# Kernel optimization log

Hardware: AMD Instinct MI355X
Metric: run time of the kernel (lower is better)

Reference implementation:

```python
import jax, jax.numpy as jnp
import numpy as np

E, H, DK, DV, HID, B, S = 512, 8, 64, 64, 2048, 8, 1024
EPS = 1e-15


def _ln(x, g, b):
    m = x.mean(-1, keepdims=True)
    v = ((x - m) ** 2).mean(-1, keepdims=True)  # unbiased=False
    return g * (x - m) / jnp.sqrt(v + EPS) + b


def _mha(x, kv, Wq, bq, Wk, bk, Wv, bv, Wo, bo, causal):
    # Wq/Wk: [H, DK, E], Wv: [H, DV, E] -- stacked per-head nn.Linear weights
    q = jnp.einsum('bse,hde->bhsd', x, Wq) + bq[None, :, None, :]
    k = jnp.einsum('bte,hde->bhtd', kv, Wk) + bk[None, :, None, :]
    v = jnp.einsum('bte,hde->bhtd', kv, Wv) + bv[None, :, None, :]
    scale = jnp.sqrt(jnp.asarray(q.shape[-1], q.dtype))
    s = jnp.einsum('bhsd,bhtd->bhst', q, k) / scale
    if causal:
        Sq, Tk = s.shape[-2], s.shape[-1]
        mask = jnp.triu(jnp.full((Sq, Tk), -jnp.inf, dtype=s.dtype), k=1)
        s = s + mask[None, None]
    p = jax.nn.softmax(s, axis=-1)
    o = jnp.einsum('bhst,bhtd->bhsd', p, v)
    b_, h_, s_, d_ = o.shape
    o = o.transpose(0, 2, 1, 3).reshape(b_, s_, h_ * d_)
    return o @ Wo.T + bo


def setup_inputs() -> dict:
    key = jax.random.key(0)
    ks = iter(jax.random.split(key, 40))

    def n(shape, s=0.02):
        return jax.random.normal(next(ks), shape, dtype=jnp.float32) * s

    inp = {
        'dec_input': jax.random.normal(next(ks), (B, S, E), dtype=jnp.float32),
        'enc_output': jax.random.normal(next(ks), (B, S, E), dtype=jnp.float32),
        # masked self-attention params
        'Wq1': n((H, DK, E)), 'bq1': jnp.zeros((H, DK), jnp.float32),
        'Wk1': n((H, DK, E)), 'bk1': jnp.zeros((H, DK), jnp.float32),
        'Wv1': n((H, DV, E)), 'bv1': jnp.zeros((H, DV), jnp.float32),
        'Wo1': n((E, H * DV)), 'bo1': jnp.zeros((E,), jnp.float32),
        # cross-attention params
        'Wq2': n((H, DK, E)), 'bq2': jnp.zeros((H, DK), jnp.float32),
        'Wk2': n((H, DK, E)), 'bk2': jnp.zeros((H, DK), jnp.float32),
        'Wv2': n((H, DV, E)), 'bv2': jnp.zeros((H, DV), jnp.float32),
        'Wo2': n((E, H * DV)), 'bo2': jnp.zeros((E,), jnp.float32),
        # feedforward params
        'Wf1': n((HID, E)), 'bf1': jnp.zeros((HID,), jnp.float32),
        'Wf2': n((E, HID)), 'bf2': jnp.zeros((E,), jnp.float32),
        # layer norm params
        'g1': jnp.ones((E,), jnp.float32), 'be1': jnp.zeros((E,), jnp.float32),
        'g2': jnp.ones((E,), jnp.float32), 'be2': jnp.zeros((E,), jnp.float32),
        'g3': jnp.ones((E,), jnp.float32), 'be3': jnp.zeros((E,), jnp.float32),
    }
    return inp


def reference(dec_input, enc_output,
              Wq1, bq1, Wk1, bk1, Wv1, bv1, Wo1, bo1,
              Wq2, bq2, Wk2, bk2, Wv2, bv2, Wo2, bo2,
              Wf1, bf1, Wf2, bf2,
              g1, be1, g2, be2, g3, be3):
    # masked multi-head self-attention + residual + norm
    a = _mha(dec_input, dec_input, Wq1, bq1, Wk1, bk1, Wv1, bv1, Wo1, bo1, True)
    x = _ln(dec_input + a, g1, be1)
    # cross-attention with encoder output + residual + norm
    c = _mha(x, enc_output, Wq2, bq2, Wk2, bk2, Wv2, bv2, Wo2, bo2, False)
    x = _ln(x + c, g2, be2)
    # position-wise feedforward + residual + norm (dropout=0 -> identity)
    f = jax.nn.relu(x @ Wf1.T + bf1) @ Wf2.T + bf2
    return _ln(x + f, g3, be3)
```

## Files before the change

### kernel.cpp

```cpp
#include <hip/hip_runtime.h>
#include <cstddef>

#define EDIM   512
#define HHEADS 8
#define DHEAD  64
#define HIDDIM 2048
#define BATCH  8
#define SEQ    1024
#define MTOK   (BATCH*SEQ)

typedef __bf16 bf16;
typedef __attribute__((ext_vector_type(8))) __bf16 bf16x8;
typedef __attribute__((ext_vector_type(4))) __bf16 bf16x4;
typedef __attribute__((ext_vector_type(4))) float f32x4;

__device__ __forceinline__ void gl_lds16(const bf16* g, bf16* l) {
  __builtin_amdgcn_global_load_lds(
      (const __attribute__((address_space(1))) unsigned int*)g,
      (__attribute__((address_space(3))) unsigned int*)l, 16, 0, 0);
}

struct WPtrs { const float* p[10]; };

__global__ __launch_bounds__(256)
void convert_weights(WPtrs w, bf16* __restrict__ dst) {
  const size_t v = ((size_t)blockIdx.x * 256 + threadIdx.x) * 4;
  const float* src;
  size_t off;
  if (v < 2097152) { src = w.p[v >> 18]; off = v & 262143; }
  else { const size_t v2 = v - 2097152; src = w.p[8 + (v2 >> 20)]; off = v2 & 1048575; }
  const float4 f = *reinterpret_cast<const float4*>(src + off);
  bf16x4 o;
  o[0] = (bf16)f.x; o[1] = (bf16)f.y; o[2] = (bf16)f.z; o[3] = (bf16)f.w;
  *reinterpret_cast<bf16x4*>(dst + v) = o;
}

__global__ __launch_bounds__(256)
void f2b_kernel(const float* __restrict__ src, bf16* __restrict__ dst) {
  const size_t i = (size_t)blockIdx.x * 256 + threadIdx.x;
  const float4 f = reinterpret_cast<const float4*>(src)[i];
  bf16x4 o;
  o[0] = (bf16)f.x; o[1] = (bf16)f.y; o[2] = (bf16)f.z; o[3] = (bf16)f.w;
  reinterpret_cast<bf16x4*>(dst)[i] = o;
}

template<int OM, bool RELU, int BN_>
__global__ __launch_bounds__(256)
void gemm_bf16(const bf16* __restrict__ A, const bf16* __restrict__ W,
               const float* __restrict__ bias, const float* __restrict__ bias2,
               const float* __restrict__ bias3,
               void* __restrict__ C0, void* __restrict__ C1, void* __restrict__ C2,
               float scale, int seg_base, int Ndim, int Kdim) {
  constexpr int WGN = BN_ / 64;
  constexpr int WGM = 4 / WGN;
  constexpr int RPW = 128 / WGM;
  constexpr int MI  = RPW / 16;
  constexpr int NI  = 4;

  __shared__ bf16 As[128 * 32];
  __shared__ bf16 Ws[BN_ * 32];
  const int tid  = threadIdx.x;
  const int lane = tid & 63;
  const int w    = tid >> 6;
  const int wr   = w / WGN, wc = w % WGN;
  const int bm   = blockIdx.y * 128;
  const int bn   = blockIdx.x * BN_;
  const int frow = lane & 15;
  const int fk   = (lane >> 4) * 8;
  const int srow = lane >> 2;
  const int scol = (lane & 3) * 8;

  f32x4 acc[MI][NI] = {};

  const int nsteps = Kdim / 32;
  for (int s = 0; s < nsteps; ++s) {
    const int k0 = s * 32;
    __syncthreads();
    gl_lds16(A + (size_t)(bm + w*16       + srow) * Kdim + k0 + scol, &As[w * 512]);
    gl_lds16(A + (size_t)(bm + (w+4)*16   + srow) * Kdim + k0 + scol, &As[(w+4) * 512]);
    gl_lds16(W + (size_t)(bn + w*16       + srow) * Kdim + k0 + scol, &Ws[w * 512]);
    if (BN_ == 128)
      gl_lds16(W + (size_t)(bn + (w+4)*16 + srow) * Kdim + k0 + scol, &Ws[(w+4) * 512]);
    __syncthreads();

    bf16x8 af[MI], wf[NI];
    #pragma unroll
    for (int mi = 0; mi < MI; ++mi)
      af[mi] = *reinterpret_cast<const bf16x8*>(&As[(wr*RPW + mi*16 + frow) * 32 + fk]);
    #pragma unroll
    for (int ni = 0; ni < NI; ++ni)
      wf[ni] = *reinterpret_cast<const bf16x8*>(&Ws[(wc*64 + ni*16 + frow) * 32 + fk]);
    #pragma unroll
    for (int mi = 0; mi < MI; ++mi)
      #pragma unroll
      for (int ni = 0; ni < NI; ++ni)
        acc[mi][ni] = __builtin_amdgcn_mfma_f32_16x16x32_bf16(
            af[mi], wf[ni], acc[mi][ni], 0, 0, 0);
  }

  const int ccol = lane & 15;
  const int crow = (lane >> 4) * 4;
  #pragma unroll
  for (int mi = 0; mi < MI; ++mi) {
    #pragma unroll
    for (int ni = 0; ni < NI; ++ni) {
      const int col  = bn + wc*64 + ni*16 + ccol;
      const int row0 = bm + wr*RPW + mi*16 + crow;
      if (OM == 0) {
        float* C = (float*)C0;
        const float bv = bias[col];
        #pragma unroll
        for (int j = 0; j < 4; ++j) {
          float vv = acc[mi][ni][j] + bv;
          if (RELU) vv = fmaxf(vv, 0.0f);
          C[(size_t)(row0 + j) * Ndim + col] = vv;
        }
      } else if (OM == 1) {
        bf16* C = (bf16*)C0;
        const float bv = bias[col];
        #pragma unroll
        for (int j = 0; j < 4; ++j) {
          float vv = acc[mi][ni][j] + bv;
          if (RELU) vv = fmaxf(vv, 0.0f);
          C[(size_t)(row0 + j) * Ndim + col] = (bf16)(vv * scale);
        }
      } else {
        const int seg = (col >> 9) + seg_base;
        const int cl  = col & 511;
        if (seg == 0) {
          bf16* C = (bf16*)C0;
          const float bv = bias[cl];
          #pragma unroll
          for (int j = 0; j < 4; ++j)
            C[(size_t)(row0 + j) * EDIM + cl] = (bf16)((acc[mi][ni][j] + bv) * scale);
        } else if (seg == 1) {
          bf16* C = (bf16*)C1;
          const float bv = bias2[cl];
          #pragma unroll
          for (int j = 0; j < 4; ++j)
            C[(size_t)(row0 + j) * EDIM + cl] = (bf16)(acc[mi][ni][j] + bv);
        } else {
          bf16* C = (bf16*)C2;
          const float bv = bias3[cl];
          bf16x4 pk;
          #pragma unroll
          for (int j = 0; j < 4; ++j) pk[j] = (bf16)(acc[mi][ni][j] + bv);
          const int bb = row0 >> 10, s0 = row0 & 1023;
          const int hh = cl >> 6,   dd = cl & 63;
          *reinterpret_cast<bf16x4*>(
              &C[((size_t)((bb * HHEADS + hh) * DHEAD + dd)) * SEQ + s0]) = pk;
        }
      }
    }
  }
}

#define APITCH 72

template<bool CAUSAL>
__global__ __launch_bounds__(256)
void attn_mfma(const bf16* __restrict__ Q, const bf16* __restrict__ K,
               const bf16* __restrict__ Vt, bf16* __restrict__ O) {
  __shared__ bf16 Ks[64][APITCH];
  __shared__ bf16 Vs[64][APITCH];
  __shared__ bf16 Pl[4][32][APITCH];

  const int qt = blockIdx.x, h = blockIdx.y, b = blockIdx.z;
  const int tid  = threadIdx.x;
  const int lane = tid & 63;
  const int w    = tid >> 6;
  const int l15  = lane & 15;
  const int lg   = lane >> 4;

  bf16x8 qf[2][2];
  #pragma unroll
  for (int t = 0; t < 2; ++t) {
    const size_t qrow = (size_t)(b * SEQ + qt * 128 + w * 32 + t * 16 + l15);
    qf[t][0] = *reinterpret_cast<const bf16x8*>(&Q[qrow * EDIM + h * DHEAD + lg * 8]);
    qf[t][1] = *reinterpret_cast<const bf16x8*>(&Q[qrow * EDIM + h * DHEAD + 32 + lg * 8]);
  }

  float m_i[2][4], l_i[2][4];
  f32x4 oacc[2][4] = {};
  #pragma unroll
  for (int t = 0; t < 2; ++t)
    #pragma unroll
    for (int r = 0; r < 4; ++r) { m_i[t][r] = -1e30f; l_i[t][r] = 0.0f; }

  const int r0 = tid >> 3;
  const int c0 = (tid & 7) * 8;
  const size_t kbase = (size_t)(b * SEQ) * EDIM + h * DHEAD;
  const size_t vbase = ((size_t)(b * HHEADS + h) * DHEAD) * SEQ;

  const int njt = CAUSAL ? (2 * qt + 2) : (SEQ / 64);

  bf16x8 pk0, pk1, pv0, pv1;
  pk0 = *reinterpret_cast<const bf16x8*>(&K[kbase + (size_t)r0 * EDIM + c0]);
  pk1 = *reinterpret_cast<const bf16x8*>(&K[kbase + (size_t)(r0 + 32) * EDIM + c0]);
  pv0 = *reinterpret_cast<const bf16x8*>(&Vt[vbase + (size_t)r0 * SEQ + c0]);
  pv1 = *reinterpret_cast<const bf16x8*>(&Vt[vbase + (size_t)(r0 + 32) * SEQ + c0]);

  for (int jt = 0; jt < njt; ++jt) {
    __syncthreads();
    *reinterpret_cast<bf16x8*>(&Ks[r0][c0])      = pk0;
    *reinterpret_cast<bf16x8*>(&Ks[r0 + 32][c0]) = pk1;
    *reinterpret_cast<bf16x8*>(&Vs[r0][c0])      = pv0;
    *reinterpret_cast<bf16x8*>(&Vs[r0 + 32][c0]) = pv1;
    __syncthreads();

    if (jt + 1 < njt) {
      const size_t ko = kbase + (size_t)((jt + 1) * 64) * EDIM;
      pk0 = *reinterpret_cast<const bf16x8*>(&K[ko + (size_t)r0 * EDIM + c0]);
      pk1 = *reinterpret_cast<const bf16x8*>(&K[ko + (size_t)(r0 + 32) * EDIM + c0]);
      const size_t vo = vbase + (size_t)(jt + 1) * 64;
      pv0 = *reinterpret_cast<const bf16x8*>(&Vt[vo + (size_t)r0 * SEQ + c0]);
      pv1 = *reinterpret_cast<const bf16x8*>(&Vt[vo + (size_t)(r0 + 32) * SEQ + c0]);
    }

    bf16x8 kf0[4], kf1[4];
    #pragma unroll
    for (int ni = 0; ni < 4; ++ni) {
      kf0[ni] = *reinterpret_cast<const bf16x8*>(&Ks[l15 + 16*ni][lg * 8]);
      kf1[ni] = *reinterpret_cast<const bf16x8*>(&Ks[l15 + 16*ni][32 + lg * 8]);
    }

    #pragma unroll
    for (int t = 0; t < 2; ++t) {
      f32x4 sf[4] = {};
      #pragma unroll
      for (int ni = 0; ni < 4; ++ni) {
        sf[ni] = __builtin_amdgcn_mfma_f32_16x16x32_bf16(qf[t][0], kf0[ni], sf[ni], 0, 0, 0);
        sf[ni] = __builtin_amdgcn_mfma_f32_16x16x32_bf16(qf[t][1], kf1[ni], sf[ni], 0, 0, 0);
      }

      if (CAUSAL && (jt + 1) * 64 > qt * 128 + w * 32 + t * 16) {
        #pragma unroll
        for (int ni = 0; ni < 4; ++ni)
          #pragma unroll
          for (int r = 0; r < 4; ++r)
            if (jt * 64 + l15 + 16*ni > qt * 128 + w * 32 + t * 16 + lg * 4 + r)
              sf[ni][r] = -1e30f;
      }

      #pragma unroll
      for (int r = 0; r < 4; ++r) {
        float rm = fmaxf(fmaxf(sf[0][r], sf[1][r]), fmaxf(sf[2][r], sf[3][r]));
        rm = fmaxf(rm, __shfl_xor(rm, 1, 16));
        rm = fmaxf(rm, __shfl_xor(rm, 2, 16));
        rm = fmaxf(rm, __shfl_xor(rm, 4, 16));
        rm = fmaxf(rm, __shfl_xor(rm, 8, 16));
        const float mn   = fmaxf(m_i[t][r], rm);
        const float corr = __expf(m_i[t][r] - mn);
        float p[4], rs = 0.0f;
        #pragma unroll
        for (int ni = 0; ni < 4; ++ni) { p[ni] = __expf(sf[ni][r] - mn); rs += p[ni]; }
        rs += __shfl_xor(rs, 1, 16); rs += __shfl_xor(rs, 2, 16);
        rs += __shfl_xor(rs, 4, 16); rs += __shfl_xor(rs, 8, 16);
        l_i[t][r] = l_i[t][r] * corr + rs;
        m_i[t][r] = mn;
        #pragma unroll
        for (int ni = 0; ni < 4; ++ni) {
          oacc[t][ni][r] *= corr;
          Pl[w][t*16 + lg*4 + r][l15 + 16*ni] = (bf16)p[ni];
        }
      }
    }

    #pragma unroll
    for (int t = 0; t < 2; ++t)
      #pragma unroll
      for (int ks = 0; ks < 2; ++ks) {
        const bf16x8 pf = *reinterpret_cast<const bf16x8*>(&Pl[w][t*16 + l15][ks*32 + lg*8]);
        #pragma unroll
        for (int ni = 0; ni < 4; ++ni) {
          const bf16x8 vf = *reinterpret_cast<const bf16x8*>(&Vs[l15 + 16*ni][ks*32 + lg*8]);
          oacc[t][ni] = __builtin_amdgcn_mfma_f32_16x16x32_bf16(pf, vf, oacc[t][ni], 0, 0, 0);
        }
      }
  }

  #pragma unroll
  for (int t = 0; t < 2; ++t)
    #pragma unroll
    for (int r = 0; r < 4; ++r) {
      const float inv = 1.0f / l_i[t][r];
      const size_t orow = (size_t)(b * SEQ + qt * 128 + w * 32 + t * 16 + lg * 4 + r);
      #pragma unroll
      for (int ni = 0; ni < 4; ++ni)
        O[orow * EDIM + h * DHEAD + l15 + 16*ni] = (bf16)(oacc[t][ni][r] * inv);
    }
}

template<bool EMITB>
__global__ __launch_bounds__(256)
void add_ln_kernel(const float* __restrict__ X, const float* __restrict__ Ain,
                   const float* __restrict__ g, const float* __restrict__ bb,
                   float* __restrict__ out, bf16* __restrict__ outb) {
  const int row = blockIdx.x;
  const int tid = threadIdx.x;
  __shared__ float red[4];
  const size_t base = (size_t)row * EDIM;

  const float v0 = X[base + tid]       + Ain[base + tid];
  const float v1 = X[base + tid + 256] + Ain[base + tid + 256];

  float s = v0 + v1;
  #pragma unroll
  for (int off = 32; off; off >>= 1) s += __shfl_down(s, off);
  if ((tid & 63) == 0) red[tid >> 6] = s;
  __syncthreads();
  const float mean = (red[0] + red[1] + red[2] + red[3]) * (1.0f / EDIM);
  __syncthreads();

  const float d0 = v0 - mean, d1 = v1 - mean;
  float vs = d0 * d0 + d1 * d1;
  #pragma unroll
  for (int off = 32; off; off >>= 1) vs += __shfl_down(vs, off);
  if ((tid & 63) == 0) red[tid >> 6] = vs;
  __syncthreads();
  const float var = (red[0] + red[1] + red[2] + red[3]) * (1.0f / EDIM);
  const float rstd = rsqrtf(var + 1e-15f);

  const float r0v = g[tid]       * (d0 * rstd) + bb[tid];
  const float r1v = g[tid + 256] * (d1 * rstd) + bb[tid + 256];
  out[base + tid]       = r0v;
  out[base + tid + 256] = r1v;
  if (EMITB) {
    outb[base + tid]       = (bf16)r0v;
    outb[base + tid + 256] = (bf16)r1v;
  }
}

extern "C" void kernel_launch(void* const* d_in, const int* in_sizes, int n_in,
                              void* d_out, int out_size, void* d_ws, size_t ws_size,
                              hipStream_t stream) {
  const float* dec = (const float*)d_in[0];
  const float* enc = (const float*)d_in[1];
  const float* Wq1 = (const float*)d_in[2];  const float* bq1 = (const float*)d_in[3];
  const float* Wk1 = (const float*)d_in[4];  const float* bk1 = (const float*)d_in[5];
  const float* Wv1 = (const float*)d_in[6];  const float* bv1 = (const float*)d_in[7];
  const float* Wo1 = (const float*)d_in[8];  const float* bo1 = (const float*)d_in[9];
  const float* Wq2 = (const float*)d_in[10]; const float* bq2 = (const float*)d_in[11];
  const float* Wk2 = (const float*)d_in[12]; const float* bk2 = (const float*)d_in[13];
  const float* Wv2 = (const float*)d_in[14]; const float* bv2 = (const float*)d_in[15];
  const float* Wo2 = (const float*)d_in[16]; const float* bo2 = (const float*)d_in[17];
  const float* Wf1 = (const float*)d_in[18]; const float* bf1 = (const float*)d_in[19];
  const float* Wf2 = (const float*)d_in[20]; const float* bf2 = (const float*)d_in[21];
  const float* g1  = (const float*)d_in[22]; const float* be1 = (const float*)d_in[23];
  const float* g2  = (const float*)d_in[24]; const float* be2 = (const float*)d_in[25];
  const float* g3  = (const float*)d_in[26]; const float* be3 = (const float*)d_in[27];
  float* out = (float*)d_out;

  char*  wsb  = (char*)d_ws;
  bf16*  decb = (bf16*)(wsb);
  bf16*  encb = (bf16*)(wsb + ((size_t)8  << 20));
  bf16*  qb   = (bf16*)(wsb + ((size_t)16 << 20));
  bf16*  kb   = (bf16*)(wsb + ((size_t)24 << 20));
  bf16*  vtb  = (bf16*)(wsb + ((size_t)32 << 20));
  bf16*  aob  = (bf16*)(wsb + ((size_t)40 << 20));
  float* x1   = (float*)(wsb + ((size_t)48 << 20));
  float* x2   = (float*)(wsb + ((size_t)64 << 20));
  float* t0   = (float*)(wsb + ((size_t)80 << 20));
  bf16*  wbf  = (bf16*)(wsb + ((size_t)96 << 20));
  bf16*  x1b  = decb;
  bf16*  x2b  = aob;
  bf16*  hidb = (bf16*)(wsb);

  bf16* wq1 = wbf + 0;
  bf16* wo1 = wbf + 786432;
  bf16* wq2 = wbf + 1048576;
  bf16* wk2 = wbf + 1310720;
  bf16* wo2 = wbf + 1835008;
  bf16* wf1 = wbf + 2097152;  bf16* wf2 = wbf + 3145728;

  const dim3 blk(256);
  const dim3 gP64(EDIM / 64, MTOK / 128);
  const dim3 gQKV(1536 / 64, MTOK / 128);
  const dim3 gKV(1024 / 64, MTOK / 128);
  const dim3 gF1(HIDDIM / 128, MTOK / 128);
  const dim3 gAttn(SEQ / 128, HHEADS, BATCH);

  WPtrs wp;
  wp.p[0] = Wq1; wp.p[1] = Wk1; wp.p[2] = Wv1; wp.p[3] = Wo1;
  wp.p[4] = Wq2; wp.p[5] = Wk2; wp.p[6] = Wv2; wp.p[7] = Wo2;
  wp.p[8] = Wf1; wp.p[9] = Wf2;
  convert_weights<<<dim3(4096), blk, 0, stream>>>(wp, wbf);
  f2b_kernel<<<dim3(4096), blk, 0, stream>>>(dec, decb);
  f2b_kernel<<<dim3(4096), blk, 0, stream>>>(enc, encb);

  gemm_bf16<3, false, 64><<<gQKV, blk, 0, stream>>>(
      decb, wq1, bq1, bk1, bv1, qb, kb, vtb, 0.125f, 0, 1536, EDIM);
  attn_mfma<true><<<gAttn, blk, 0, stream>>>(qb, kb, vtb, aob);
  gemm_bf16<0, false, 64><<<gP64, blk, 0, stream>>>(
      aob, wo1, bo1, nullptr, nullptr, t0, nullptr, nullptr, 1.0f, 0, EDIM, EDIM);
  add_ln_kernel<true><<<dim3(MTOK), blk, 0, stream>>>(dec, t0, g1, be1, x1, x1b);

  gemm_bf16<1, false, 64><<<gP64, blk, 0, stream>>>(
      x1b, wq2, bq2, nullptr, nullptr, qb, nullptr, nullptr, 0.125f, 0, EDIM, EDIM);
  gemm_bf16<3, false, 64><<<gKV, blk, 0, stream>>>(
      encb, wk2, nullptr, bk2, bv2, nullptr, kb, vtb, 1.0f, 1, 1024, EDIM);
  attn_mfma<false><<<gAttn, blk, 0, stream>>>(qb, kb, vtb, aob);
  gemm_bf16<0, false, 64><<<gP64, blk, 0, stream>>>(
      aob, wo2, bo2, nullptr, nullptr, t0, nullptr, nullptr, 1.0f, 0, EDIM, EDIM);
  add_ln_kernel<true><<<dim3(MTOK), blk, 0, stream>>>(x1, t0, g2, be2, x2, x2b);

  gemm_bf16<1, true, 128><<<gF1, blk, 0, stream>>>(
      x2b, wf1, bf1, nullptr, nullptr, hidb, nullptr, nullptr, 1.0f, 0, HIDDIM, EDIM);
  gemm_bf16<0, false, 64><<<gP64, blk, 0, stream>>>(
      hidb, wf2, bf2, nullptr, nullptr, t0, nullptr, nullptr, 1.0f, 0, EDIM, HIDDIM);
  add_ln_kernel<false><<<dim3(MTOK), blk, 0, stream>>>(x2, t0, g3, be3, out, nullptr);

  (void)in_sizes; (void)n_in; (void)out_size; (void)ws_size;
}
```

Measured before the change: 480.6 us.

## Double-buffer GEMM with K=64 swizzled LDS tiles and shrink attention query tiles

The GEMM now loads K-slices of 64 into two LDS buffers, prefetching the next tile with async global-to-LDS loads while computing the current one. It uses an XOR swizzle to avoid bank conflicts and a single 128x64 tile shape, dropping the BN=128 variant for FF1. The attention kernel now processes 64 query rows per block (16 per wave) instead of 128, doubling the grid and simplifying the causal mask to the diagonal tile only. The aim is to overlap memory latency with MFMA work, cut LDS conflicts and improve occupancy and load balance, at the cost of more LDS per block and more K/V reloads in attention.

```diff
diff --git a/kernel.cpp b/kernel.cpp
--- a/kernel.cpp
+++ b/kernel.cpp
@@ -44,58 +44,81 @@
   reinterpret_cast<bf16x4*>(dst)[i] = o;
 }
 
-template<int OM, bool RELU, int BN_>
+template<int OM, bool RELU>
 __global__ __launch_bounds__(256)
 void gemm_bf16(const bf16* __restrict__ A, const bf16* __restrict__ W,
                const float* __restrict__ bias, const float* __restrict__ bias2,
                const float* __restrict__ bias3,
                void* __restrict__ C0, void* __restrict__ C1, void* __restrict__ C2,
                float scale, int seg_base, int Ndim, int Kdim) {
-  constexpr int WGN = BN_ / 64;
-  constexpr int WGM = 4 / WGN;
-  constexpr int RPW = 128 / WGM;
-  constexpr int MI  = RPW / 16;
-  constexpr int NI  = 4;
-
-  __shared__ bf16 As[128 * 32];
-  __shared__ bf16 Ws[BN_ * 32];
+  constexpr int MI = 2, NI = 4;
+
+  __shared__ bf16 As[2][128 * 64];
+  __shared__ bf16 Ws[2][64 * 64];
   const int tid  = threadIdx.x;
   const int lane = tid & 63;
   const int w    = tid >> 6;
-  const int wr   = w / WGN, wc = w % WGN;
   const int bm   = blockIdx.y * 128;
-  const int bn   = blockIdx.x * BN_;
+  const int bn   = blockIdx.x * 64;
   const int frow = lane & 15;
-  const int fk   = (lane >> 4) * 8;
-  const int srow = lane >> 2;
-  const int scol = (lane & 3) * 8;
+  const int lg   = lane >> 4;
+  const int srow = lane >> 3;
+  const int scol = ((lane & 7) ^ srow) * 8;
+  const bf16* Ag = A + (size_t)bm * Kdim;
+  const bf16* Wg = W + (size_t)bn * Kdim;
 
   f32x4 acc[MI][NI] = {};
 
-  const int nsteps = Kdim / 32;
+  const int nsteps = Kdim / 64;
+
+  #pragma unroll
+  for (int c = 0; c < 4; ++c)
+    gl_lds16(Ag + (size_t)((w + c*4)*8 + srow) * Kdim + scol, &As[0][(w + c*4) * 512]);
+  #pragma unroll
+  for (int c = 0; c < 2; ++c)
+    gl_lds16(Wg + (size_t)((w + c*4)*8 + srow) * Kdim + scol, &Ws[0][(w + c*4) * 512]);
+  __syncthreads();
+
   for (int s = 0; s < nsteps; ++s) {
-    const int k0 = s * 32;
+    const int cur = s & 1;
+    if (s + 1 < nsteps) {
+      const int k0 = (s + 1) * 64;
+      #pragma unroll
+      for (int c = 0; c < 4; ++c)
+        gl_lds16(Ag + (size_t)((w + c*4)*8 + srow) * Kdim + k0 + scol,
+                 &As[cur ^ 1][(w + c*4) * 512]);
+      #pragma unroll
+      for (int c = 0; c < 2; ++c)
+        gl_lds16(Wg + (size_t)((w + c*4)*8 + srow) * Kdim + k0 + scol,
+                 &Ws[cur ^ 1][(w + c*4) * 512]);
+    }
+
+    bf16x8 af[MI][2], wf[NI][2];
+    #pragma unroll
+    for (int mi = 0; mi < MI; ++mi)
+      #pragma unroll
+      for (int kk = 0; kk < 2; ++kk) {
+        const int row  = w*32 + mi*16 + frow;
+        const int phys = (kk*4 + lg) ^ (frow & 7);
+        af[mi][kk] = *reinterpret_cast<const bf16x8*>(&As[cur][row*64 + phys*8]);
+      }
+    #pragma unroll
+    for (int ni = 0; ni < NI; ++ni)
+      #pragma unroll
+      for (int kk = 0; kk < 2; ++kk) {
+        const int row  = ni*16 + frow;
+        const int phys = (kk*4 + lg) ^ (frow & 7);
+        wf[ni][kk] = *reinterpret_cast<const bf16x8*>(&Ws[cur][row*64 + phys*8]);
+      }
+    #pragma unroll
+    for (int kk = 0; kk < 2; ++kk)
+      #pragma unroll
+      for (int mi = 0; mi < MI; ++mi)
+        #pragma unroll
+        for (int ni = 0; ni < NI; ++ni)
+          acc[mi][ni] = __builtin_amdgcn_mfma_f32_16x16x32_bf16(
+              af[mi][kk], wf[ni][kk], acc[mi][ni], 0, 0, 0);
     __syncthreads();
-    gl_lds16(A + (size_t)(bm + w*16       + srow) * Kdim + k0 + scol, &As[w * 512]);
-    gl_lds16(A + (size_t)(bm + (w+4)*16   + srow) * Kdim + k0 + scol, &As[(w+4) * 512]);
-    gl_lds16(W + (size_t)(bn + w*16       + srow) * Kdim + k0 + scol, &Ws[w * 512]);
-    if (BN_ == 128)
-      gl_lds16(W + (size_t)(bn + (w+4)*16 + srow) * Kdim + k0 + scol, &Ws[(w+4) * 512]);
-    __syncthreads();
-
-    bf16x8 af[MI], wf[NI];
-    #pragma unroll
-    for (int mi = 0; mi < MI; ++mi)
-      af[mi] = *reinterpret_cast<const bf16x8*>(&As[(wr*RPW + mi*16 + frow) * 32 + fk]);
-    #pragma unroll
-    for (int ni = 0; ni < NI; ++ni)
-      wf[ni] = *reinterpret_cast<const bf16x8*>(&Ws[(wc*64 + ni*16 + frow) * 32 + fk]);
-    #pragma unroll
-    for (int mi = 0; mi < MI; ++mi)
-      #pragma unroll
-      for (int ni = 0; ni < NI; ++ni)
-        acc[mi][ni] = __builtin_amdgcn_mfma_f32_16x16x32_bf16(
-            af[mi], wf[ni], acc[mi][ni], 0, 0, 0);
   }
 
   const int ccol = lane & 15;
@@ -104,8 +127,8 @@
   for (int mi = 0; mi < MI; ++mi) {
     #pragma unroll
     for (int ni = 0; ni < NI; ++ni) {
-      const int col  = bn + wc*64 + ni*16 + ccol;
-      const int row0 = bm + wr*RPW + mi*16 + crow;
+      const int col  = bn + ni*16 + ccol;
+      const int row0 = bm + w*32 + mi*16 + crow;
       if (OM == 0) {
         float* C = (float*)C0;
         const float bv = bias[col];
@@ -163,7 +186,7 @@
                const bf16* __restrict__ Vt, bf16* __restrict__ O) {
   __shared__ bf16 Ks[64][APITCH];
   __shared__ bf16 Vs[64][APITCH];
-  __shared__ bf16 Pl[4][32][APITCH];
+  __shared__ bf16 Pl[4][16][APITCH];
 
   const int qt = blockIdx.x, h = blockIdx.y, b = blockIdx.z;
   const int tid  = threadIdx.x;
@@ -172,27 +195,21 @@
   const int l15  = lane & 15;
   const int lg   = lane >> 4;
 
-  bf16x8 qf[2][2];
-  #pragma unroll
-  for (int t = 0; t < 2; ++t) {
-    const size_t qrow = (size_t)(b * SEQ + qt * 128 + w * 32 + t * 16 + l15);
-    qf[t][0] = *reinterpret_cast<const bf16x8*>(&Q[qrow * EDIM + h * DHEAD + lg * 8]);
-    qf[t][1] = *reinterpret_cast<const bf16x8*>(&Q[qrow * EDIM + h * DHEAD + 32 + lg * 8]);
-  }
-
-  float m_i[2][4], l_i[2][4];
-  f32x4 oacc[2][4] = {};
-  #pragma unroll
-  for (int t = 0; t < 2; ++t)
-    #pragma unroll
-    for (int r = 0; r < 4; ++r) { m_i[t][r] = -1e30f; l_i[t][r] = 0.0f; }
+  const size_t qrow = (size_t)(b * SEQ + qt * 64 + w * 16 + l15);
+  const bf16x8 qf0 = *reinterpret_cast<const bf16x8*>(&Q[qrow * EDIM + h * DHEAD + lg * 8]);
+  const bf16x8 qf1 = *reinterpret_cast<const bf16x8*>(&Q[qrow * EDIM + h * DHEAD + 32 + lg * 8]);
+
+  float m_i[4], l_i[4];
+  f32x4 oacc[4] = {};
+  #pragma unroll
+  for (int r = 0; r < 4; ++r) { m_i[r] = -1e30f; l_i[r] = 0.0f; }
 
   const int r0 = tid >> 3;
   const int c0 = (tid & 7) * 8;
   const size_t kbase = (size_t)(b * SEQ) * EDIM + h * DHEAD;
   const size_t vbase = ((size_t)(b * HHEADS + h) * DHEAD) * SEQ;
 
-  const int njt = CAUSAL ? (2 * qt + 2) : (SEQ / 64);
+  const int njt = CAUSAL ? (qt + 1) : (SEQ / 64);
 
   bf16x8 pk0, pk1, pv0, pv1;
   pk0 = *reinterpret_cast<const bf16x8*>(&K[kbase + (size_t)r0 * EDIM + c0]);
@@ -217,78 +234,65 @@
       pv1 = *reinterpret_cast<const bf16x8*>(&Vt[vo + (size_t)(r0 + 32) * SEQ + c0]);
     }
 
-    bf16x8 kf0[4], kf1[4];
+    f32x4 sf[4] = {};
     #pragma unroll
     for (int ni = 0; ni < 4; ++ni) {
-      kf0[ni] = *reinterpret_cast<const bf16x8*>(&Ks[l15 + 16*ni][lg * 8]);
-      kf1[ni] = *reinterpret_cast<const bf16x8*>(&Ks[l15 + 16*ni][32 + lg * 8]);
-    }
-
-    #pragma unroll
-    for (int t = 0; t < 2; ++t) {
-      f32x4 sf[4] = {};
+      const bf16x8 kf0 = *reinterpret_cast<const bf16x8*>(&Ks[l15 + 16*ni][lg * 8]);
+      const bf16x8 kf1 = *reinterpret_cast<const bf16x8*>(&Ks[l15 + 16*ni][32 + lg * 8]);
+      sf[ni] = __builtin_amdgcn_mfma_f32_16x16x32_bf16(qf0, kf0, sf[ni], 0, 0, 0);
+      sf[ni] = __builtin_amdgcn_mfma_f32_16x16x32_bf16(qf1, kf1, sf[ni], 0, 0, 0);
+    }
+
+    if (CAUSAL && jt == qt) {
+      #pragma unroll
+      for (int ni = 0; ni < 4; ++ni)
+        #pragma unroll
+        for (int r = 0; r < 4; ++r)
+          if (l15 + 16*ni > w*16 + lg*4 + r) sf[ni][r] = -1e30f;
+    }
+
+    #pragma unroll
+    for (int r = 0; r < 4; ++r) {
+      float rm = fmaxf(fmaxf(sf[0][r], sf[1][r]), fmaxf(sf[2][r], sf[3][r]));
+      rm = fmaxf(rm, __shfl_xor(rm, 1, 16));
+      rm = fmaxf(rm, __shfl_xor(rm, 2, 16));
+      rm = fmaxf(rm, __shfl_xor(rm, 4, 16));
+      rm = fmaxf(rm, __shfl_xor(rm, 8, 16));
+      const float mn   = fmaxf(m_i[r], rm);
+      const float corr = __expf(m_i[r] - mn);
+      float p[4], rs = 0.0f;
+      #pragma unroll
+      for (int ni = 0; ni < 4; ++ni) { p[ni] = __expf(sf[ni][r] - mn); rs += p[ni]; }
+      rs += __shfl_xor(rs, 1, 16); rs += __shfl_xor(rs, 2, 16);
+      rs += __shfl_xor(rs, 4, 16); rs += __shfl_xor(rs, 8, 16);
+      l_i[r] = l_i[r] * corr + rs;
+      m_i[r] = mn;
       #pragma unroll
       for (int ni = 0; ni < 4; ++ni) {
-        sf[ni] = __builtin_amdgcn_mfma_f32_16x16x32_bf16(qf[t][0], kf0[ni], sf[ni], 0, 0, 0);
-        sf[ni] = __builtin_amdgcn_mfma_f32_16x16x32_bf16(qf[t][1], kf1[ni], sf[ni], 0, 0, 0);
+        oacc[ni][r] *= corr;
+        Pl[w][lg*4 + r][l15 + 16*ni] = (bf16)p[ni];
       }
-
-      if (CAUSAL && (jt + 1) * 64 > qt * 128 + w * 32 + t * 16) {
-        #pragma unroll
-        for (int ni = 0; ni < 4; ++ni)
-          #pragma unroll
-          for (int r = 0; r < 4; ++r)
-            if (jt * 64 + l15 + 16*ni > qt * 128 + w * 32 + t * 16 + lg * 4 + r)
-              sf[ni][r] = -1e30f;
+    }
+
+    #pragma unroll
+    for (int ks = 0; ks < 2; ++ks) {
+      const bf16x8 pf = *reinterpret_cast<const bf16x8*>(&Pl[w][l15][ks*32 + lg*8]);
+      #pragma unroll
+      for (int ni = 0; ni < 4; ++ni) {
+        const bf16x8 vf = *reinterpret_cast<const bf16x8*>(&Vs[l15 + 16*ni][ks*32 + lg*8]);
+        oacc[ni] = __builtin_amdgcn_mfma_f32_16x16x32_bf16(pf, vf, oacc[ni], 0, 0, 0);
       }
-
-      #pragma unroll
-      for (int r = 0; r < 4; ++r) {
-        float rm = fmaxf(fmaxf(sf[0][r], sf[1][r]), fmaxf(sf[2][r], sf[3][r]));
-        rm = fmaxf(rm, __shfl_xor(rm, 1, 16));
-        rm = fmaxf(rm, __shfl_xor(rm, 2, 16));
-        rm = fmaxf(rm, __shfl_xor(rm, 4, 16));
-        rm = fmaxf(rm, __shfl_xor(rm, 8, 16));
-        const float mn   = fmaxf(m_i[t][r], rm);
-        const float corr = __expf(m_i[t][r] - mn);
-        float p[4], rs = 0.0f;
-        #pragma unroll
-        for (int ni = 0; ni < 4; ++ni) { p[ni] = __expf(sf[ni][r] - mn); rs += p[ni]; }
-        rs += __shfl_xor(rs, 1, 16); rs += __shfl_xor(rs, 2, 16);
-        rs += __shfl_xor(rs, 4, 16); rs += __shfl_xor(rs, 8, 16);
-        l_i[t][r] = l_i[t][r] * corr + rs;
-        m_i[t][r] = mn;
-        #pragma unroll
-        for (int ni = 0; ni < 4; ++ni) {
-          oacc[t][ni][r] *= corr;
-          Pl[w][t*16 + lg*4 + r][l15 + 16*ni] = (bf16)p[ni];
-        }
-      }
-    }
-
-    #pragma unroll
-    for (int t = 0; t < 2; ++t)
-      #pragma unroll
-      for (int ks = 0; ks < 2; ++ks) {
-        const bf16x8 pf = *reinterpret_cast<const bf16x8*>(&Pl[w][t*16 + l15][ks*32 + lg*8]);
-        #pragma unroll
-        for (int ni = 0; ni < 4; ++ni) {
-          const bf16x8 vf = *reinterpret_cast<const bf16x8*>(&Vs[l15 + 16*ni][ks*32 + lg*8]);
-          oacc[t][ni] = __builtin_amdgcn_mfma_f32_16x16x32_bf16(pf, vf, oacc[t][ni], 0, 0, 0);
-        }
-      }
+    }
   }
 
   #pragma unroll
-  for (int t = 0; t < 2; ++t)
-    #pragma unroll
-    for (int r = 0; r < 4; ++r) {
-      const float inv = 1.0f / l_i[t][r];
-      const size_t orow = (size_t)(b * SEQ + qt * 128 + w * 32 + t * 16 + lg * 4 + r);
-      #pragma unroll
-      for (int ni = 0; ni < 4; ++ni)
-        O[orow * EDIM + h * DHEAD + l15 + 16*ni] = (bf16)(oacc[t][ni][r] * inv);
-    }
+  for (int r = 0; r < 4; ++r) {
+    const float inv = 1.0f / l_i[r];
+    const size_t orow = (size_t)(b * SEQ + qt * 64 + w * 16 + lg * 4 + r);
+    #pragma unroll
+    for (int ni = 0; ni < 4; ++ni)
+      O[orow * EDIM + h * DHEAD + l15 + 16*ni] = (bf16)(oacc[ni][r] * inv);
+  }
 }
 
 template<bool EMITB>
@@ -377,8 +381,8 @@
   const dim3 gP64(EDIM / 64, MTOK / 128);
   const dim3 gQKV(1536 / 64, MTOK / 128);
   const dim3 gKV(1024 / 64, MTOK / 128);
-  const dim3 gF1(HIDDIM / 128, MTOK / 128);
-  const dim3 gAttn(SEQ / 128, HHEADS, BATCH);
+  const dim3 gF1(HIDDIM / 64, MTOK / 128);
+  const dim3 gAttn(SEQ / 64, HHEADS, BATCH);
 
   WPtrs wp;
   wp.p[0] = Wq1; wp.p[1] = Wk1; wp.p[2] = Wv1; wp.p[3] = Wo1;
@@ -388,25 +392,25 @@
   f2b_kernel<<<dim3(4096), blk, 0, stream>>>(dec, decb);
   f2b_kernel<<<dim3(4096), blk, 0, stream>>>(enc, encb);
 
-  gemm_bf16<3, false, 64><<<gQKV, blk, 0, stream>>>(
+  gemm_bf16<3, false><<<gQKV, blk, 0, stream>>>(
       decb, wq1, bq1, bk1, bv1, qb, kb, vtb, 0.125f, 0, 1536, EDIM);
   attn_mfma<true><<<gAttn, blk, 0, stream>>>(qb, kb, vtb, aob);
-  gemm_bf16<0, false, 64><<<gP64, blk, 0, stream>>>(
+  gemm_bf16<0, false><<<gP64, blk, 0, stream>>>(
       aob, wo1, bo1, nullptr, nullptr, t0, nullptr, nullptr, 1.0f, 0, EDIM, EDIM);
   add_ln_kernel<true><<<dim3(MTOK), blk, 0, stream>>>(dec, t0, g1, be1, x1, x1b);
 
-  gemm_bf16<1, false, 64><<<gP64, blk, 0, stream>>>(
+  gemm_bf16<1, false><<<gP64, blk, 0, stream>>>(
       x1b, wq2, bq2, nullptr, nullptr, qb, nullptr, nullptr, 0.125f, 0, EDIM, EDIM);
-  gemm_bf16<3, false, 64><<<gKV, blk, 0, stream>>>(
+  gemm_bf16<3, false><<<gKV, blk, 0, stream>>>(
       encb, wk2, nullptr, bk2, bv2, nullptr, kb, vtb, 1.0f, 1, 1024, EDIM);
   attn_mfma<false><<<gAttn, blk, 0, stream>>>(qb, kb, vtb, aob);
-  gemm_bf16<0, false, 64><<<gP64, blk, 0, stream>>>(
+  gemm_bf16<0, false><<<gP64, blk, 0, stream>>>(
       aob, wo2, bo2, nullptr, nullptr, t0, nullptr, nullptr, 1.0f, 0, EDIM, EDIM);
   add_ln_kernel<true><<<dim3(MTOK), blk, 0, stream>>>(x1, t0, g2, be2, x2, x2b);
 
-  gemm_bf16<1, true, 128><<<gF1, blk, 0, stream>>>(
+  gemm_bf16<1, true><<<gF1, blk, 0, stream>>>(
       x2b, wf1, bf1, nullptr, nullptr, hidb, nullptr, nullptr, 1.0f, 0, HIDDIM, EDIM);
-  gemm_bf16<0, false, 64><<<gP64, blk, 0, stream>>>(
+  gemm_bf16<0, false><<<gP64, blk, 0, stream>>>(
       hidb, wf2, bf2, nullptr, nullptr, t0, nullptr, nullptr, 1.0f, 0, EDIM, HIDDIM);
   add_ln_kernel<false><<<dim3(MTOK), blk, 0, stream>>>(x2, t0, g3, be3, out, nullptr);
 
```

After: 456.3 us. 5.1% less time.
